# Performance work log

Hardware: AMD Instinct MI355X
Metric: run time of the kernel (lower is better)

Reference implementation:

```python
import jax, jax.numpy as jnp
import numpy as np

N = 50000
E = 640000
M = 400000
D_IN, H1, H2, H3, D_OUT = 256, 128, 128, 64, 32


def _glorot(key, shape, gain=1.0):
    fan_in, fan_out = shape[0], shape[1]
    lim = gain * np.sqrt(6.0 / (fan_in + fan_out))
    return jax.random.uniform(key, shape, jnp.float32, -lim, lim)


def setup_inputs() -> dict:
    key = jax.random.key(0)
    ks = jax.random.split(key, 16)
    x = jax.random.normal(ks[0], (N, D_IN), jnp.float32)
    edge_index = jax.random.randint(ks[1], (2, E), 0, N, jnp.int64)
    train_sample = jax.random.randint(ks[2], (M, 2), 0, N, jnp.int64)
    g = 1.414
    return {
        "x": x,
        "edge_index": edge_index,
        "train_sample": train_sample,
        "W1": _glorot(ks[3], (D_IN, H1)),
        "W2": _glorot(ks[4], (H1, H2)),
        "tf_w1": _glorot(ks[5], (H2, H3), g), "tf_b1": jnp.zeros((H3,), jnp.float32),
        "tf_w2": _glorot(ks[6], (H3, D_OUT), g), "tf_b2": jnp.zeros((D_OUT,), jnp.float32),
        "tg_w1": _glorot(ks[7], (H2, H3), g), "tg_b1": jnp.zeros((H3,), jnp.float32),
        "tg_w2": _glorot(ks[8], (H3, D_OUT), g), "tg_b2": jnp.zeros((D_OUT,), jnp.float32),
    }


def _gcn_conv(x, W, src, dst, norm, n):
    # GCNConv (no bias): out = D^-1/2 (A+I) D^-1/2 (x @ W)
    h = x @ W
    msg = h[src] * norm[:, None]          # [E+N, H]
    return jax.ops.segment_sum(msg, dst, num_segments=n)


def reference(x, edge_index, train_sample, W1, W2, tf_w1, tf_b1, tf_w2, tf_b2, tg_w1, tg_b1, tg_w2, tg_b2):
    n = x.shape[0]
    loop = jnp.arange(n, dtype=edge_index.dtype)
    src = jnp.concatenate([edge_index[0], loop])
    dst = jnp.concatenate([edge_index[1], loop])
    deg = jnp.zeros((n,), x.dtype).at[dst].add(1.0)
    dis = jax.lax.rsqrt(deg)              # deg >= 1 due to self loops
    norm = dis[src] * dis[dst]

    # encode
    h = jax.nn.elu(_gcn_conv(x, W1, src, dst, norm, n))
    embed = _gcn_conv(h, W2, src, dst, norm, n)

    # tf / target MLP branches (dropout p=0.01 treated as identity)
    lrelu = jax.nn.leaky_relu
    tf = lrelu(lrelu(embed @ tf_w1 + tf_b1) @ tf_w2 + tf_b2)
    tg = lrelu(lrelu(embed @ tg_w1 + tg_b1) @ tg_w2 + tg_b2)

    # gather + dot decode
    t = tf[train_sample[:, 0]]
    u = tg[train_sample[:, 1]]
    return jnp.sum(t * u, axis=1, keepdims=True)  # [M,1]
```

## Files before the change

kernel.cpp:

```cpp
#include <hip/hip_runtime.h>
#include <hip/hip_bf16.h>
#include <math.h>


typedef __attribute__((ext_vector_type(8))) short short8v;
typedef __attribute__((ext_vector_type(4))) float f32x4;

__device__ inline unsigned short f2bf_rne(float f) {
    unsigned u = __float_as_uint(f);
    unsigned r = u + 0x7FFFu + ((u >> 16) & 1u);
    return (unsigned short)(r >> 16);
}
__device__ inline float bf2f(unsigned short h) {
    return __uint_as_float(((unsigned)h) << 16);
}

__global__ void zero_ideg_kernel(int* __restrict__ ideg, int n) {
    int i = blockIdx.x * 256 + threadIdx.x;
    if (i < n) ideg[i] = 0;
}

__global__ void ideg_accum_kernel(int* __restrict__ ideg, const int* __restrict__ dst, int e) {
    int i = blockIdx.x * 256 + threadIdx.x;
    if (i < e) atomicAdd(&ideg[dst[i]], 1);
}

__global__ __launch_bounds__(256) void scan_blk_kernel(const int* __restrict__ ideg,
                                                       int* __restrict__ row_ptr,
                                                       float* __restrict__ dis,
                                                       int* __restrict__ partials, int n) {
    __shared__ int wsum[4];
    const int t = threadIdx.x;
    const int lane = t & 63;
    const int wid = t >> 6;
    const int i0 = blockIdx.x * 1024 + t * 4;
    int4 v = make_int4(0, 0, 0, 0);
    if (i0 + 3 < n) {
        v = *(const int4*)&ideg[i0];
    } else if (i0 < n) {
        v.x = ideg[i0];
        if (i0 + 1 < n) v.y = ideg[i0 + 1];
        if (i0 + 2 < n) v.z = ideg[i0 + 2];
    }
    if (i0 < n) {
        dis[i0] = rsqrtf(1.f + (float)v.x);
        if (i0 + 1 < n) dis[i0 + 1] = rsqrtf(1.f + (float)v.y);
        if (i0 + 2 < n) dis[i0 + 2] = rsqrtf(1.f + (float)v.z);
        if (i0 + 3 < n) dis[i0 + 3] = rsqrtf(1.f + (float)v.w);
    }
    int s = v.x + v.y + v.z + v.w;
    int incl = s;
#pragma unroll
    for (int off = 1; off < 64; off <<= 1) {
        int tv = __shfl_up(incl, off, 64);
        if (lane >= off) incl += tv;
    }
    if (lane == 63) wsum[wid] = incl;
    __syncthreads();
    if (t == 0) {
        int a = 0;
#pragma unroll
        for (int ww = 0; ww < 4; ++ww) { int tmp = wsum[ww]; wsum[ww] = a; a += tmp; }
    }
    __syncthreads();
    int ex = wsum[wid] + incl - s;
    if (i0 < n) {
        row_ptr[i0] = ex;
        if (i0 + 1 < n) row_ptr[i0 + 1] = ex + v.x;
        if (i0 + 2 < n) row_ptr[i0 + 2] = ex + v.x + v.y;
        if (i0 + 3 < n) row_ptr[i0 + 3] = ex + v.x + v.y + v.z;
    }
    if (t == 255) partials[blockIdx.x] = wsum[3] + incl;
}

__global__ void scan_part_kernel(int* __restrict__ partials, int nb) {
    int lane = threadIdx.x;
    int v = (lane < nb) ? partials[lane] : 0;
    int incl = v;
#pragma unroll
    for (int off = 1; off < 64; off <<= 1) {
        int tv = __shfl_up(incl, off, 64);
        if (lane >= off) incl += tv;
    }
    if (lane < nb) partials[lane] = incl - v;
}

__global__ void scan_add_kernel(int* __restrict__ row_ptr, const int* __restrict__ partials, int n) {
    int i = blockIdx.x * 256 + threadIdx.x;
    if (i < n) row_ptr[i] += partials[i >> 10];
}

__global__ void fill_kernel(const int* __restrict__ src, const int* __restrict__ dst,
                            int* __restrict__ row_ptr, int* __restrict__ csr, int e) {
    int i = blockIdx.x * 256 + threadIdx.x;
    if (i < e) {
        int d = dst[i];
        int pos = atomicAdd(&row_ptr[d], 1);
        csr[pos] = src[i];
    }
}

__global__ void prep_weights_kernel(
    const float* __restrict__ W1, const float* __restrict__ W2,
    const float* __restrict__ tfw1, const float* __restrict__ tfb1,
    const float* __restrict__ tfw2, const float* __restrict__ tfb2,
    const float* __restrict__ tgw1, const float* __restrict__ tgb1,
    const float* __restrict__ tgw2, const float* __restrict__ tgb2,
    unsigned short* __restrict__ wf,
    float* __restrict__ bcat1, float* __restrict__ bcat2)
{
    int id = blockIdx.x * 256 + threadIdx.x;
    if (id >= 147456) {
        if (id < 147456 + 128) {
            int c = id - 147456;
            bcat1[c] = (c < 64) ? tfb1[c] : tgb1[c - 64];
        } else if (id < 147456 + 192) {
            int c = id - 147456 - 128;
            bcat2[c] = (c < 32) ? tfb2[c] : tgb2[c - 32];
        }
        return;
    }
    int base, NF;
    int lid;
    if (id < 65536)       { base = 0;      NF = 8; lid = id; }
    else if (id < 98304)  { base = 65536;  NF = 8; lid = id - 65536; }
    else if (id < 131072) { base = 98304;  NF = 8; lid = id - 98304; }
    else                  { base = 131072; NF = 4; lid = id - 131072; }

    int j    = lid & 7;
    int lane = (lid >> 3) & 63;
    int h    = (lid >> 9) & 1;
    int rest = lid >> 10;
    int c    = rest % NF;
    int kk   = rest / NF;
    int k    = kk * 32 + (lane >> 4) * 8 + j;
    int col  = c * 16 + (lane & 15);

    float w;
    if (id < 65536) {
        w = W1[k * 128 + col];
    } else if (id < 98304) {
        w = W2[k * 128 + col];
    } else if (id < 131072) {
        w = (col < 64) ? tfw1[k * 64 + col] : tgw1[k * 64 + (col - 64)];
    } else {
        w = 0.f;
        if (k < 64 && col < 32) w = tfw2[k * 32 + col];
        else if (k >= 64 && col >= 32) w = tgw2[(k - 64) * 32 + (col - 32)];
    }
    unsigned short hb = f2bf_rne(w);
    wf[base + lid] = h ? f2bf_rne(w - bf2f(hb)) : hb;
}

template <int K, int NCOL, bool ELU_IN, bool LRELU, bool BIAS>
__global__ __launch_bounds__(256) void mfma_gemm_kernel(
    const float* __restrict__ X, const unsigned short* __restrict__ wf,
    const float* __restrict__ bias, float* __restrict__ Y, int nrows)
{
    constexpr int NF = NCOL / 16;
    constexpr int NK = K / 32;

    const int t = threadIdx.x;
    const int lane = t & 63;
    const int w = t >> 6;
    const int row0 = blockIdx.x * 64 + w * 16;

    const int arow = row0 + (lane & 15);
    const bool rowok = arow < nrows;
    const float* xrow = X + (size_t)arow * K + ((lane >> 4) * 8);

    f32x4 acc[NF];
#pragma unroll
    for (int c = 0; c < NF; ++c) acc[c] = (f32x4){0.f, 0.f, 0.f, 0.f};

#pragma unroll 2
    for (int kk = 0; kk < NK; ++kk) {
        float4 v0 = make_float4(0.f, 0.f, 0.f, 0.f);
        float4 v1 = v0;
        if (rowok) {
            v0 = *(const float4*)&xrow[kk * 32];
            v1 = *(const float4*)&xrow[kk * 32 + 4];
        }
        if (ELU_IN) {
            v0.x = (v0.x > 0.f) ? v0.x : expm1f(v0.x);
            v0.y = (v0.y > 0.f) ? v0.y : expm1f(v0.y);
            v0.z = (v0.z > 0.f) ? v0.z : expm1f(v0.z);
            v0.w = (v0.w > 0.f) ? v0.w : expm1f(v0.w);
            v1.x = (v1.x > 0.f) ? v1.x : expm1f(v1.x);
            v1.y = (v1.y > 0.f) ? v1.y : expm1f(v1.y);
            v1.z = (v1.z > 0.f) ? v1.z : expm1f(v1.z);
            v1.w = (v1.w > 0.f) ? v1.w : expm1f(v1.w);
        }
        float a[8] = {v0.x, v0.y, v0.z, v0.w, v1.x, v1.y, v1.z, v1.w};
        short8v ah, al;
#pragma unroll
        for (int j = 0; j < 8; ++j) {
            unsigned short hb = f2bf_rne(a[j]);
            ah[j] = (short)hb;
            al[j] = (short)f2bf_rne(a[j] - bf2f(hb));
        }
        const unsigned short* wfk = wf + (size_t)(kk * NF * 2) * 512 + lane * 8;
        short8v bh[NF], bl[NF];
#pragma unroll
        for (int c = 0; c < NF; ++c) {
            bh[c] = *(const short8v*)(wfk + (c * 2 + 0) * 512);
            bl[c] = *(const short8v*)(wfk + (c * 2 + 1) * 512);
        }
#pragma unroll
        for (int c = 0; c < NF; ++c) {
            acc[c] = __builtin_amdgcn_mfma_f32_16x16x32_bf16(ah, bh[c], acc[c], 0, 0, 0);
            acc[c] = __builtin_amdgcn_mfma_f32_16x16x32_bf16(al, bh[c], acc[c], 0, 0, 0);
            acc[c] = __builtin_amdgcn_mfma_f32_16x16x32_bf16(ah, bl[c], acc[c], 0, 0, 0);
        }
    }

#pragma unroll
    for (int c = 0; c < NF; ++c) {
        int gcol = c * 16 + (lane & 15);
        float bv = BIAS ? bias[gcol] : 0.f;
#pragma unroll
        for (int q = 0; q < 4; ++q) {
            int grow = row0 + (lane >> 4) * 4 + q;
            if (grow < nrows) {
                float o = acc[c][q] + bv;
                if (LRELU) o = (o > 0.f) ? o : 0.01f * o;
                Y[(size_t)grow * NCOL + gcol] = o;
            }
        }
    }
}

__global__ __launch_bounds__(256) void gather_kernel(const float* __restrict__ h,
                                                     const int* __restrict__ row_ptr,
                                                     const int* __restrict__ csr,
                                                     const float* __restrict__ dis,
                                                     float* __restrict__ outp, int n) {
    int node = blockIdx.x * 8 + (threadIdx.x >> 5);
    int l = threadIdx.x & 31;
    if (node >= n) return;
    int beg = (node == 0) ? 0 : row_ptr[node - 1];
    int end = row_ptr[node];
    float dd = dis[node];
    const float4* h4 = (const float4*)h;
    float4 self = h4[(size_t)node * 32 + l];
    float ax = self.x * dd, ay = self.y * dd, az = self.z * dd, aw = self.w * dd;
    int j = beg;
    for (; j + 4 <= end; j += 4) {
        int s0 = csr[j + 0], s1 = csr[j + 1], s2 = csr[j + 2], s3 = csr[j + 3];
        float d0 = dis[s0], d1 = dis[s1], d2 = dis[s2], d3 = dis[s3];
        float4 v0 = h4[(size_t)s0 * 32 + l];
        float4 v1 = h4[(size_t)s1 * 32 + l];
        float4 v2 = h4[(size_t)s2 * 32 + l];
        float4 v3 = h4[(size_t)s3 * 32 + l];
        ax += v0.x * d0 + v1.x * d1 + v2.x * d2 + v3.x * d3;
        ay += v0.y * d0 + v1.y * d1 + v2.y * d2 + v3.y * d3;
        az += v0.z * d0 + v1.z * d1 + v2.z * d2 + v3.z * d3;
        aw += v0.w * d0 + v1.w * d1 + v2.w * d2 + v3.w * d3;
    }
    for (; j < end; ++j) {
        int s = csr[j];
        float ds = dis[s];
        float4 v = h4[(size_t)s * 32 + l];
        ax += v.x * ds; ay += v.y * ds; az += v.z * ds; aw += v.w * ds;
    }
    float4 o;
    o.x = ax * dd; o.y = ay * dd; o.z = az * dd; o.w = aw * dd;
    ((float4*)outp)[(size_t)node * 32 + l] = o;
}

__global__ void dot_kernel(const float* __restrict__ Z,
                           const int* __restrict__ ts, float* __restrict__ out, int m) {
    int gid = blockIdx.x * 256 + threadIdx.x;
    int s = gid >> 3;
    int l = gid & 7;
    if (s >= m) return;
    int ti = ts[2 * s + 0];
    int ui = ts[2 * s + 1];
    float4 a = *(const float4*)&Z[(size_t)ti * 64 + l * 4];
    float4 b = *(const float4*)&Z[(size_t)ui * 64 + 32 + l * 4];
    float d = a.x * b.x + a.y * b.y + a.z * b.z + a.w * b.w;
    d += __shfl_down(d, 4, 8);
    d += __shfl_down(d, 2, 8);
    d += __shfl_down(d, 1, 8);
    if (l == 0) out[s] = d;
}

extern "C" void kernel_launch(void* const* d_in, const int* in_sizes, int n_in,
                              void* d_out, int out_size, void* d_ws, size_t ws_size,
                              hipStream_t stream) {
    const float* x     = (const float*)d_in[0];
    const int*   ei    = (const int*)d_in[1];
    const int*   ts    = (const int*)d_in[2];
    const float* W1    = (const float*)d_in[3];
    const float* W2    = (const float*)d_in[4];
    const float* tf_w1 = (const float*)d_in[5];
    const float* tf_b1 = (const float*)d_in[6];
    const float* tf_w2 = (const float*)d_in[7];
    const float* tf_b2 = (const float*)d_in[8];
    const float* tg_w1 = (const float*)d_in[9];
    const float* tg_b1 = (const float*)d_in[10];
    const float* tg_w2 = (const float*)d_in[11];
    const float* tg_b2 = (const float*)d_in[12];
    float* out = (float*)d_out;

    const int n = in_sizes[0] / 256;
    const int e = in_sizes[1] / 2;
    const int m = in_sizes[2] / 2;
    const int* src = ei;
    const int* dstp = ei + e;

    float* wsf = (float*)d_ws;
    float* dis     = wsf;
    int*   row_ptr = (int*)(wsf + 50176);
    int*   partials = row_ptr + 50048;
    int*   ideg    = (int*)(wsf + 100352);
    int*   csr     = (int*)(wsf + 100352);
    unsigned short* wfrag = (unsigned short*)(wsf + 740416);
    unsigned short* w1f = wfrag;
    unsigned short* w2f = wfrag + 65536;
    unsigned short* h1f = wfrag + 98304;
    unsigned short* h2f = wfrag + 131072;
    float* bcat1 = wsf + 740416 + 73728;
    float* bcat2 = wsf + 814272;
    float* A = wsf + 814336;
    float* B = A + (size_t)n * 128;
    float* C = B + (size_t)n * 128;

    const int nb_n = (n + 255) / 256;
    const int nb_e = (e + 255) / 256;
    const int nsb  = (n + 1023) / 1024;
    const int gg   = (n + 7) / 8;
    const int gm   = (n + 63) / 64;

    zero_ideg_kernel<<<nb_n, 256, 0, stream>>>(ideg, n);
    ideg_accum_kernel<<<nb_e, 256, 0, stream>>>(ideg, dstp, e);
    scan_blk_kernel<<<nsb, 256, 0, stream>>>(ideg, row_ptr, dis, partials, n);
    scan_part_kernel<<<1, 64, 0, stream>>>(partials, nsb);
    scan_add_kernel<<<nb_n, 256, 0, stream>>>(row_ptr, partials, n);
    fill_kernel<<<nb_e, 256, 0, stream>>>(src, dstp, row_ptr, csr, e);

    prep_weights_kernel<<<(147648 + 255) / 256, 256, 0, stream>>>(
        W1, W2, tf_w1, tf_b1, tf_w2, tf_b2, tg_w1, tg_b1, tg_w2, tg_b2,
        wfrag, bcat1, bcat2);

    mfma_gemm_kernel<256, 128, false, false, false><<<gm, 256, 0, stream>>>(x, w1f, nullptr, A, n);
    gather_kernel<<<gg, 256, 0, stream>>>(A, row_ptr, csr, dis, B, n);

    mfma_gemm_kernel<128, 128, true, false, false><<<gm, 256, 0, stream>>>(B, w2f, nullptr, C, n);
    gather_kernel<<<gg, 256, 0, stream>>>(C, row_ptr, csr, dis, A, n);

    mfma_gemm_kernel<128, 128, false, true, true><<<gm, 256, 0, stream>>>(A, h1f, bcat1, B, n);
    mfma_gemm_kernel<128, 64, false, true, true><<<gm, 256, 0, stream>>>(B, h2f, bcat2, C, n);

    dot_kernel<<<(m * 8 + 255) / 256, 256, 0, stream>>>(C, ts, out, m);
}
```

Before: 363.5 us.

## Fuse two MLP head GEMMs via LDS and batch CSR index loads in gather

Replaces the two separate head GEMM launches with one kernel. It keeps the first layer's leaky-ReLU output in shared memory as split bf16 hi/lo and feeds it straight into the second MFMA GEMM, so the 50000x128 intermediate never makes a round trip through global memory. The gather kernel now loads up to 32 neighbor indices and their dis values cooperatively, one per lane, then broadcasts them with shuffles, instead of having every lane redundantly load csr and dis. The cost is extra LDS use and a loop structure that depends on degree.

After: 354.4 us. -2.5%, faster.

```diff
diff --git a/kernel.cpp b/kernel.cpp
--- a/kernel.cpp
+++ b/kernel.cpp
@@ -230,6 +230,110 @@
     }
 }
 
+__global__ __launch_bounds__(256) void fused_heads_kernel(
+    const float* __restrict__ X, const unsigned short* __restrict__ h1f,
+    const unsigned short* __restrict__ h2f, const float* __restrict__ bcat1,
+    const float* __restrict__ bcat2, float* __restrict__ Z, int nrows)
+{
+    constexpr int LDT = 136;
+    __shared__ unsigned short t1h[4][16][LDT];
+    __shared__ unsigned short t1l[4][16][LDT];
+
+    const int t = threadIdx.x;
+    const int lane = t & 63;
+    const int w = t >> 6;
+    const int row0 = blockIdx.x * 64 + w * 16;
+
+    const int arow = row0 + (lane & 15);
+    const bool rowok = arow < nrows;
+    const float* xrow = X + (size_t)arow * 128 + ((lane >> 4) * 8);
+
+    f32x4 acc[8];
+#pragma unroll
+    for (int c = 0; c < 8; ++c) acc[c] = (f32x4){0.f, 0.f, 0.f, 0.f};
+
+#pragma unroll 2
+    for (int kk = 0; kk < 4; ++kk) {
+        float4 v0 = make_float4(0.f, 0.f, 0.f, 0.f);
+        float4 v1 = v0;
+        if (rowok) {
+            v0 = *(const float4*)&xrow[kk * 32];
+            v1 = *(const float4*)&xrow[kk * 32 + 4];
+        }
+        float a[8] = {v0.x, v0.y, v0.z, v0.w, v1.x, v1.y, v1.z, v1.w};
+        short8v ah, al;
+#pragma unroll
+        for (int j = 0; j < 8; ++j) {
+            unsigned short hb = f2bf_rne(a[j]);
+            ah[j] = (short)hb;
+            al[j] = (short)f2bf_rne(a[j] - bf2f(hb));
+        }
+        const unsigned short* wfk = h1f + (size_t)(kk * 16) * 512 + lane * 8;
+        short8v bh[8], bl[8];
+#pragma unroll
+        for (int c = 0; c < 8; ++c) {
+            bh[c] = *(const short8v*)(wfk + (c * 2 + 0) * 512);
+            bl[c] = *(const short8v*)(wfk + (c * 2 + 1) * 512);
+        }
+#pragma unroll
+        for (int c = 0; c < 8; ++c) {
+            acc[c] = __builtin_amdgcn_mfma_f32_16x16x32_bf16(ah, bh[c], acc[c], 0, 0, 0);
+            acc[c] = __builtin_amdgcn_mfma_f32_16x16x32_bf16(al, bh[c], acc[c], 0, 0, 0);
+            acc[c] = __builtin_amdgcn_mfma_f32_16x16x32_bf16(ah, bl[c], acc[c], 0, 0, 0);
+        }
+    }
+
+#pragma unroll
+    for (int c = 0; c < 8; ++c) {
+        int col = c * 16 + (lane & 15);
+        float bv = bcat1[col];
+#pragma unroll
+        for (int q = 0; q < 4; ++q) {
+            int r = (lane >> 4) * 4 + q;
+            float o = acc[c][q] + bv;
+            o = (o > 0.f) ? o : 0.01f * o;
+            unsigned short hb = f2bf_rne(o);
+            t1h[w][r][col] = hb;
+            t1l[w][r][col] = f2bf_rne(o - bf2f(hb));
+        }
+    }
+
+    f32x4 acc2[4];
+#pragma unroll
+    for (int c = 0; c < 4; ++c) acc2[c] = (f32x4){0.f, 0.f, 0.f, 0.f};
+
+#pragma unroll
+    for (int kk = 0; kk < 4; ++kk) {
+        int koff = kk * 32 + (lane >> 4) * 8;
+        short8v ah = *(const short8v*)&t1h[w][lane & 15][koff];
+        short8v al = *(const short8v*)&t1l[w][lane & 15][koff];
+        const unsigned short* wfk = h2f + (size_t)(kk * 8) * 512 + lane * 8;
+#pragma unroll
+        for (int c = 0; c < 4; ++c) {
+            short8v bh = *(const short8v*)(wfk + (c * 2 + 0) * 512);
+            short8v bl = *(const short8v*)(wfk + (c * 2 + 1) * 512);
+            acc2[c] = __builtin_amdgcn_mfma_f32_16x16x32_bf16(ah, bh, acc2[c], 0, 0, 0);
+            acc2[c] = __builtin_amdgcn_mfma_f32_16x16x32_bf16(al, bh, acc2[c], 0, 0, 0);
+            acc2[c] = __builtin_amdgcn_mfma_f32_16x16x32_bf16(ah, bl, acc2[c], 0, 0, 0);
+        }
+    }
+
+#pragma unroll
+    for (int c = 0; c < 4; ++c) {
+        int gcol = c * 16 + (lane & 15);
+        float bv = bcat2[gcol];
+#pragma unroll
+        for (int q = 0; q < 4; ++q) {
+            int grow = row0 + (lane >> 4) * 4 + q;
+            if (grow < nrows) {
+                float o = acc2[c][q] + bv;
+                o = (o > 0.f) ? o : 0.01f * o;
+                Z[(size_t)grow * 64 + gcol] = o;
+            }
+        }
+    }
+}
+
 __global__ __launch_bounds__(256) void gather_kernel(const float* __restrict__ h,
                                                      const int* __restrict__ row_ptr,
                                                      const int* __restrict__ csr,
@@ -244,24 +348,33 @@
     const float4* h4 = (const float4*)h;
     float4 self = h4[(size_t)node * 32 + l];
     float ax = self.x * dd, ay = self.y * dd, az = self.z * dd, aw = self.w * dd;
-    int j = beg;
-    for (; j + 4 <= end; j += 4) {
-        int s0 = csr[j + 0], s1 = csr[j + 1], s2 = csr[j + 2], s3 = csr[j + 3];
-        float d0 = dis[s0], d1 = dis[s1], d2 = dis[s2], d3 = dis[s3];
-        float4 v0 = h4[(size_t)s0 * 32 + l];
-        float4 v1 = h4[(size_t)s1 * 32 + l];
-        float4 v2 = h4[(size_t)s2 * 32 + l];
-        float4 v3 = h4[(size_t)s3 * 32 + l];
-        ax += v0.x * d0 + v1.x * d1 + v2.x * d2 + v3.x * d3;
-        ay += v0.y * d0 + v1.y * d1 + v2.y * d2 + v3.y * d3;
-        az += v0.z * d0 + v1.z * d1 + v2.z * d2 + v3.z * d3;
-        aw += v0.w * d0 + v1.w * d1 + v2.w * d2 + v3.w * d3;
-    }
-    for (; j < end; ++j) {
-        int s = csr[j];
-        float ds = dis[s];
-        float4 v = h4[(size_t)s * 32 + l];
-        ax += v.x * ds; ay += v.y * ds; az += v.z * ds; aw += v.w * ds;
+
+    for (int j0 = beg; j0 < end; j0 += 32) {
+        int cnt = end - j0; if (cnt > 32) cnt = 32;
+        int idx = 0;
+        if (j0 + l < end) idx = csr[j0 + l];
+        float dsv = dis[idx];
+        int k = 0;
+        for (; k + 4 <= cnt; k += 4) {
+            int s0 = __shfl(idx, k + 0, 32), s1 = __shfl(idx, k + 1, 32);
+            int s2 = __shfl(idx, k + 2, 32), s3 = __shfl(idx, k + 3, 32);
+            float d0 = __shfl(dsv, k + 0, 32), d1 = __shfl(dsv, k + 1, 32);
+            float d2 = __shfl(dsv, k + 2, 32), d3 = __shfl(dsv, k + 3, 32);
+            float4 v0 = h4[(size_t)s0 * 32 + l];
+            float4 v1 = h4[(size_t)s1 * 32 + l];
+            float4 v2 = h4[(size_t)s2 * 32 + l];
+            float4 v3 = h4[(size_t)s3 * 32 + l];
+            ax += v0.x * d0 + v1.x * d1 + v2.x * d2 + v3.x * d3;
+            ay += v0.y * d0 + v1.y * d1 + v2.y * d2 + v3.y * d3;
+            az += v0.z * d0 + v1.z * d1 + v2.z * d2 + v3.z * d3;
+            aw += v0.w * d0 + v1.w * d1 + v2.w * d2 + v3.w * d3;
+        }
+        for (; k < cnt; ++k) {
+            int s = __shfl(idx, k, 32);
+            float ds = __shfl(dsv, k, 32);
+            float4 v = h4[(size_t)s * 32 + l];
+            ax += v.x * ds; ay += v.y * ds; az += v.z * ds; aw += v.w * ds;
+        }
     }
     float4 o;
     o.x = ax * dd; o.y = ay * dd; o.z = az * dd; o.w = aw * dd;
@@ -349,8 +462,7 @@
     mfma_gemm_kernel<128, 128, true, false, false><<<gm, 256, 0, stream>>>(B, w2f, nullptr, C, n);
     gather_kernel<<<gg, 256, 0, stream>>>(C, row_ptr, csr, dis, A, n);
 
-    mfma_gemm_kernel<128, 128, false, true, true><<<gm, 256, 0, stream>>>(A, h1f, bcat1, B, n);
-    mfma_gemm_kernel<128, 64, false, true, true><<<gm, 256, 0, stream>>>(B, h2f, bcat2, C, n);
+    fused_heads_kernel<<<gm, 256, 0, stream>>>(A, h1f, h2f, bcat1, bcat2, C, n);
 
     dot_kernel<<<(m * 8 + 255) / 256, 256, 0, stream>>>(C, ts, out, m);
 }
```
